# Kernel tuning notes

Measured on AMD Instinct MI355X. Metric: run time of the kernel, lower is better.

Reference implementation:

```python
import jax, jax.numpy as jnp
import numpy as np
import math

DIM = 1024
HEADS = 16
HEAD_DIM = DIM // HEADS
EXPERTS = 8
HIDDEN = 4096  # mlp_ratio * dim
TOP_K = 2
CAP_FACTOR = 1.25
B, S = 2, 2048
CAPACITY = int(math.ceil(B * S * TOP_K * CAP_FACTOR / EXPERTS))  # 1280
EPS = 1e-6


def setup_inputs() -> dict:
    key = jax.random.key(0)
    ks = jax.random.split(key, 16)
    sc_d = 1.0 / math.sqrt(DIM)
    sc_h = 1.0 / math.sqrt(HIDDEN)
    return {
        "x": jax.random.normal(ks[0], (B, S, DIM), jnp.float32),
        "cos": jax.random.uniform(ks[1], (S, HEAD_DIM), jnp.float32),
        "sin": jax.random.uniform(ks[2], (S, HEAD_DIM), jnp.float32),
        "ln1_g": jnp.ones((DIM,), jnp.float32),
        "ln1_b": jnp.zeros((DIM,), jnp.float32),
        "ln2_g": jnp.ones((DIM,), jnp.float32),
        "ln2_b": jnp.zeros((DIM,), jnp.float32),
        "wqkv": jax.random.normal(ks[3], (DIM, 3 * DIM), jnp.float32) * sc_d,
        "bqkv": jnp.zeros((3 * DIM,), jnp.float32),
        "wo": jax.random.normal(ks[4], (DIM, DIM), jnp.float32) * sc_d,
        "bo": jnp.zeros((DIM,), jnp.float32),
        "gate_w": jax.random.normal(ks[5], (DIM, EXPERTS), jnp.float32) * sc_d,
        "w1": jax.random.normal(ks[6], (EXPERTS, DIM, HIDDEN), jnp.float32) * sc_d,
        "b1": jnp.zeros((EXPERTS, HIDDEN), jnp.float32),
        "w2": jax.random.normal(ks[7], (EXPERTS, HIDDEN, DIM), jnp.float32) * sc_h,
        "b2": jnp.zeros((EXPERTS, DIM), jnp.float32),
    }


def _layernorm(x, g, b):
    mu = jnp.mean(x, -1, keepdims=True)
    var = jnp.var(x, -1, keepdims=True)
    return (x - mu) * jax.lax.rsqrt(var + EPS) * g + b


def _rope(t, cos, sin):
    # t: [B, H, S, Dh]; cos/sin: [S, Dh]
    d = t.shape[-1] // 2
    t1, t2 = t[..., :d], t[..., d:]
    rot = jnp.concatenate([-t2, t1], axis=-1)
    return t * cos + rot * sin


def _attention(h, cos, sin, wqkv, bqkv, wo, bo):
    b, s, d = h.shape
    qkv = h @ wqkv + bqkv
    q, k, v = jnp.split(qkv, 3, axis=-1)
    def heads(t):
        return t.reshape(b, s, HEADS, HEAD_DIM).transpose(0, 2, 1, 3)
    q, k, v = heads(q), heads(k), heads(v)
    q = _rope(q, cos, sin)
    k = _rope(k, cos, sin)
    scores = jnp.einsum("bhqd,bhkd->bhqk", q, k) / math.sqrt(HEAD_DIM)
    attn = jax.nn.softmax(scores, axis=-1)
    o = jnp.einsum("bhqk,bhkd->bhqd", attn, v)
    o = o.transpose(0, 2, 1, 3).reshape(b, s, d)
    return o @ wo + bo


def _moe(h, gate_w, w1, b1, w2, b2):
    b, s, d = h.shape
    T = b * s
    xt = h.reshape(T, d)
    probs = jax.nn.softmax(xt @ gate_w, axis=-1)  # [T, E]
    topv, topi = jax.lax.top_k(probs, TOP_K)      # [T, K]
    topw = topv / jnp.sum(topv, -1, keepdims=True)
    # k-major flatten so all first-choice routes get priority
    eid = topi.T.reshape(-1)                      # [K*T]
    wflat = topw.T.reshape(-1)
    tok = jnp.tile(jnp.arange(T), TOP_K)
    oh = jax.nn.one_hot(eid, EXPERTS, dtype=jnp.float32)
    pos = (jnp.cumsum(oh, axis=0) * oh - oh).sum(-1).astype(jnp.int32)
    keep = (pos < CAPACITY).astype(xt.dtype)
    posc = jnp.minimum(pos, CAPACITY - 1)
    buf = jnp.zeros((EXPERTS, CAPACITY, d), xt.dtype).at[eid, posc].add(xt[tok] * keep[:, None])
    hh = jax.nn.gelu(jnp.einsum("ecd,edh->ech", buf, w1) + b1[:, None, :])
    out = jnp.einsum("ech,ehd->ecd", hh, w2) + b2[:, None, :]
    yflat = out[eid, posc] * (wflat * keep)[:, None]
    y = jnp.zeros_like(xt).at[tok].add(yflat)
    # load-balancing aux loss
    me = jnp.mean(probs, axis=0)
    ce = jnp.mean(jax.nn.one_hot(topi, EXPERTS, dtype=jnp.float32).sum(1), axis=0) / TOP_K
    aux = EXPERTS * jnp.sum(me * ce)
    return y.reshape(b, s, d), aux


def reference(x, cos, sin, ln1_g, ln1_b, ln2_g, ln2_b, wqkv, bqkv, wo, bo,
              gate_w, w1, b1, w2, b2):
    h = _layernorm(x, ln1_g, ln1_b)
    x = x + _attention(h, cos, sin, wqkv, bqkv, wo, bo)
    h2 = _layernorm(x, ln2_g, ln2_b)
    y, aux = _moe(h2, gate_w, w1, b1, w2, b2)
    return x + y, aux
```

## Files before the change

kernel.cpp:

```cpp
#include <hip/hip_runtime.h>


typedef unsigned short u16;
typedef short bf16x8 __attribute__((ext_vector_type(8)));
typedef float f32x4 __attribute__((ext_vector_type(4)));
typedef _Float16 f16;
typedef f16 f16x8 __attribute__((ext_vector_type(8)));
typedef f16 f16x4 __attribute__((ext_vector_type(4)));
typedef f16 f16x2 __attribute__((ext_vector_type(2)));

#define T_TOKENS 4096
#define SEQ      2048
#define CAPACITY 1280

__device__ __forceinline__ u16 f2bf(float f) {
  unsigned int u = __float_as_uint(f);
  return (u16)((u + 0x7FFFu + ((u >> 16) & 1u)) >> 16);
}
__device__ __forceinline__ float bf2f(u16 h) {
  return __uint_as_float(((unsigned int)h) << 16);
}
__device__ __forceinline__ float gelu_f(float x) {
  float x3 = x * x * x;
  float t = tanhf(0.7978845608028654f * (x + 0.044715f * x3));
  return 0.5f * x * (1.0f + t);
}

__global__ __launch_bounds__(256) void ln_kernel(
    const float* __restrict__ x, const float* __restrict__ g,
    const float* __restrict__ bt, float* __restrict__ of32,
    u16* __restrict__ obf, f16* __restrict__ oh, f16* __restrict__ ol) {
  const int t = blockIdx.x, tid = threadIdx.x;
  float4 v = ((const float4*)(x + (size_t)t * 1024))[tid];
  float s = v.x + v.y + v.z + v.w;
  float sq = v.x * v.x + v.y * v.y + v.z * v.z + v.w * v.w;
#pragma unroll
  for (int d = 1; d < 64; d <<= 1) {
    s += __shfl_xor(s, d);
    sq += __shfl_xor(sq, d);
  }
  __shared__ float red[8];
  if ((tid & 63) == 0) { red[tid >> 6] = s; red[4 + (tid >> 6)] = sq; }
  __syncthreads();
  s = red[0] + red[1] + red[2] + red[3];
  sq = red[4] + red[5] + red[6] + red[7];
  const float mu = s * (1.0f / 1024.0f);
  const float var = sq * (1.0f / 1024.0f) - mu * mu;
  const float rs = rsqrtf(var + 1e-6f);
  float4 gv = ((const float4*)g)[tid];
  float4 bv = ((const float4*)bt)[tid];
  float4 o;
  o.x = (v.x - mu) * rs * gv.x + bv.x;
  o.y = (v.y - mu) * rs * gv.y + bv.y;
  o.z = (v.z - mu) * rs * gv.z + bv.z;
  o.w = (v.w - mu) * rs * gv.w + bv.w;
  if (of32) ((float4*)(of32 + (size_t)t * 1024))[tid] = o;
  if (obf) {
    ushort4 ob;
    ob.x = f2bf(o.x); ob.y = f2bf(o.y); ob.z = f2bf(o.z); ob.w = f2bf(o.w);
    ((ushort4*)(obf + (size_t)t * 1024))[tid] = ob;
  }
  if (oh) {
    const float f[4] = {o.x, o.y, o.z, o.w};
    f16x4 hv, lv;
#pragma unroll
    for (int i = 0; i < 4; ++i) {
      f16 hi = (f16)f[i];
      hv[i] = hi;
      lv[i] = (f16)(f[i] - (float)hi);
    }
    ((f16x4*)(oh + (size_t)t * 1024))[tid] = hv;
    ((f16x4*)(ol + (size_t)t * 1024))[tid] = lv;
  }
}

__global__ __launch_bounds__(256) void transpose_f32_f16hl(
    const float* __restrict__ in, f16* __restrict__ outh, f16* __restrict__ outl,
    int R, int C) {
  __shared__ float tile[32][33];
  const int c0 = blockIdx.x * 32, r0 = blockIdx.y * 32;
  const int tx = threadIdx.x & 31, ty = threadIdx.x >> 5;
#pragma unroll
  for (int i = 0; i < 32; i += 8)
    tile[ty + i][tx] = in[(size_t)(r0 + ty + i) * C + c0 + tx];
  __syncthreads();
#pragma unroll
  for (int i = 0; i < 32; i += 8) {
    const float v = tile[tx][ty + i];
    const f16 hi = (f16)v;
    const size_t idx = (size_t)(c0 + ty + i) * R + r0 + tx;
    outh[idx] = hi;
    outl[idx] = (f16)(v - (float)hi);
  }
}

template <int EPI>
__global__ __launch_bounds__(256, 2) void gemm_f16x3_bt(
    const f16* __restrict__ Agh, const f16* __restrict__ Agl,
    const f16* __restrict__ Bth, const f16* __restrict__ Btl,
    const float* __restrict__ bias, const float* __restrict__ res,
    float* __restrict__ C, f16* __restrict__ Ch, f16* __restrict__ Cl,
    int M, int N, int K) {
  __shared__ f16 Ah[128 * 40], Al[128 * 40], Bh[128 * 40], Bl[128 * 40];
  const int tid = threadIdx.x, lane = tid & 63, w = tid >> 6;
  const int qd = lane >> 4, ml = lane & 15;
  const int m0 = blockIdx.y * 128, n0 = blockIdx.x * 128;
  const int wm = (w & 1) * 64, wn = (w >> 1) * 64;
  f32x4 acc[4][4] = {};

  const int sr = tid >> 1, sc = (tid & 1) * 16;
  const f16* gAh = Agh + (size_t)(m0 + sr) * K + sc;
  const f16* gAl = Agl + (size_t)(m0 + sr) * K + sc;
  const f16* gBh = Bth + (size_t)(n0 + sr) * K + sc;
  const f16* gBl = Btl + (size_t)(n0 + sr) * K + sc;
  f16* lAh = &Ah[sr * 40 + sc];
  f16* lAl = &Al[sr * 40 + sc];
  f16* lBh = &Bh[sr * 40 + sc];
  f16* lBl = &Bl[sr * 40 + sc];

  for (int k0 = 0; k0 < K; k0 += 32) {
    const uint4 ah0 = *(const uint4*)(gAh + k0);
    const uint4 ah1 = *(const uint4*)(gAh + k0 + 8);
    const uint4 al0 = *(const uint4*)(gAl + k0);
    const uint4 al1 = *(const uint4*)(gAl + k0 + 8);
    const uint4 bh0 = *(const uint4*)(gBh + k0);
    const uint4 bh1 = *(const uint4*)(gBh + k0 + 8);
    const uint4 bl0 = *(const uint4*)(gBl + k0);
    const uint4 bl1 = *(const uint4*)(gBl + k0 + 8);
    __syncthreads();
    *(uint4*)lAh = ah0; *(uint4*)(lAh + 8) = ah1;
    *(uint4*)lAl = al0; *(uint4*)(lAl + 8) = al1;
    *(uint4*)lBh = bh0; *(uint4*)(lBh + 8) = bh1;
    *(uint4*)lBl = bl0; *(uint4*)(lBl + 8) = bl1;
    __syncthreads();
    f16x8 fah[4], fal[4], fbh[4], fbl[4];
#pragma unroll
    for (int i = 0; i < 4; ++i) {
      fah[i] = *(const f16x8*)&Ah[(wm + i * 16 + ml) * 40 + qd * 8];
      fal[i] = *(const f16x8*)&Al[(wm + i * 16 + ml) * 40 + qd * 8];
    }
#pragma unroll
    for (int j = 0; j < 4; ++j) {
      fbh[j] = *(const f16x8*)&Bh[(wn + j * 16 + ml) * 40 + qd * 8];
      fbl[j] = *(const f16x8*)&Bl[(wn + j * 16 + ml) * 40 + qd * 8];
    }
#pragma unroll
    for (int i = 0; i < 4; ++i)
#pragma unroll
      for (int j = 0; j < 4; ++j) {
        acc[i][j] = __builtin_amdgcn_mfma_f32_16x16x32_f16(fah[i], fbh[j], acc[i][j], 0, 0, 0);
        acc[i][j] = __builtin_amdgcn_mfma_f32_16x16x32_f16(fah[i], fbl[j], acc[i][j], 0, 0, 0);
        acc[i][j] = __builtin_amdgcn_mfma_f32_16x16x32_f16(fal[i], fbh[j], acc[i][j], 0, 0, 0);
      }
  }
#pragma unroll
  for (int i = 0; i < 4; ++i) {
    const int rr = m0 + wm + i * 16 + qd * 4;
#pragma unroll
    for (int j = 0; j < 4; ++j) {
      const int cc = n0 + wn + j * 16 + ml;
      const float bb = bias[cc];
#pragma unroll
      for (int p = 0; p < 4; ++p) {
        float v = acc[i][j][p] + bb;
        const size_t idx = (size_t)(rr + p) * N + cc;
        if (EPI == 1) {
          C[idx] = v + res[idx];
        } else {
          const f16 hi = (f16)v;
          Ch[idx] = hi;
          Cl[idx] = (f16)(v - (float)hi);
        }
      }
    }
  }
}

__global__ __launch_bounds__(256) void rope_kernel(
    f16* __restrict__ qh, f16* __restrict__ ql, const float* __restrict__ cosb,
    const float* __restrict__ sinb) {
  const int t = blockIdx.x;
  const int s = t & (SEQ - 1);
  f16* rh = qh + (size_t)t * 3072;
  f16* rl = ql + (size_t)t * 3072;
  const int tid = threadIdx.x;
#pragma unroll
  for (int it = 0; it < 2; ++it) {
    const int p = tid + it * 256;
    const int sec = p >> 8;
    const int rem = p & 255;
    const int hd = rem >> 4, d = (rem & 15) * 2;
    const int col = sec * 1024 + hd * 64 + d;
    const float c1a = cosb[s * 64 + d], s1a = sinb[s * 64 + d];
    const float c1b = cosb[s * 64 + d + 1], s1b = sinb[s * 64 + d + 1];
    const float c2a = cosb[s * 64 + d + 32], s2a = sinb[s * 64 + d + 32];
    const float c2b = cosb[s * 64 + d + 33], s2b = sinb[s * 64 + d + 33];
    const f16x2 ah = *(const f16x2*)(rh + col);
    const f16x2 al = *(const f16x2*)(rl + col);
    const f16x2 bh = *(const f16x2*)(rh + col + 32);
    const f16x2 bl = *(const f16x2*)(rl + col + 32);
    const float a0 = (float)ah[0] + (float)al[0];
    const float a1 = (float)ah[1] + (float)al[1];
    const float b0 = (float)bh[0] + (float)bl[0];
    const float b1 = (float)bh[1] + (float)bl[1];
    float na0 = a0 * c1a - b0 * s1a;
    float na1 = a1 * c1b - b1 * s1b;
    float nb0 = b0 * c2a + a0 * s2a;
    float nb1 = b1 * c2b + a1 * s2b;
    if (sec == 0) { na0 *= 0.125f; na1 *= 0.125f; nb0 *= 0.125f; nb1 *= 0.125f; }
    f16x2 nah, nal, nbh, nbl;
    nah[0] = (f16)na0; nal[0] = (f16)(na0 - (float)nah[0]);
    nah[1] = (f16)na1; nal[1] = (f16)(na1 - (float)nah[1]);
    nbh[0] = (f16)nb0; nbl[0] = (f16)(nb0 - (float)nbh[0]);
    nbh[1] = (f16)nb1; nbl[1] = (f16)(nb1 - (float)nbh[1]);
    *(f16x2*)(rh + col) = nah;
    *(f16x2*)(rl + col) = nal;
    *(f16x2*)(rh + col + 32) = nbh;
    *(f16x2*)(rl + col + 32) = nbl;
  }
}

__global__ __launch_bounds__(256) void attn_mfma(
    const f16* __restrict__ qkvh, const f16* __restrict__ qkvl,
    f16* __restrict__ ogh, f16* __restrict__ ogl) {
  const int bh_ = blockIdx.y, b = bh_ >> 4, h = bh_ & 15;
  const int tid = threadIdx.x, w = tid >> 6, lane = tid & 63;
  const int quad = lane >> 4, ml = lane & 15;
  const int q0 = blockIdx.x * 64;
  const f16* baseh = qkvh + (size_t)b * SEQ * 3072 + h * 64;
  const f16* basel = qkvl + (size_t)b * SEQ * 3072 + h * 64;

  __shared__ f16 Kh[64 * 72], Kl[64 * 72];
  __shared__ f16 Vh[64 * 72], Vl[64 * 72];
  __shared__ f16 Ph[64 * 72], Pl[64 * 72];

  f16x8 qh[2], ql[2];
  {
    const f16* qrh = baseh + (size_t)(q0 + w * 16 + ml) * 3072;
    const f16* qrl = basel + (size_t)(q0 + w * 16 + ml) * 3072;
#pragma unroll
    for (int ks = 0; ks < 2; ++ks) {
      qh[ks] = *(const f16x8*)(qrh + ks * 32 + quad * 8);
      ql[ks] = *(const f16x8*)(qrl + ks * 32 + quad * 8);
    }
  }

  float m_i[4] = {-1e30f, -1e30f, -1e30f, -1e30f};
  float l_i[4] = {0.f, 0.f, 0.f, 0.f};
  f32x4 accO[4] = {};

  const int skey = tid >> 2, scg = (tid & 3) * 16;
  const int sd0 = (tid & 15) * 4, sk0 = (tid >> 4) * 4;

  for (int c0 = 0; c0 < SEQ; c0 += 64) {
    __syncthreads();
    {
      const f16* krh = baseh + 1024 + (size_t)(c0 + skey) * 3072 + scg;
      const f16* krl = basel + 1024 + (size_t)(c0 + skey) * 3072 + scg;
      *(f16x8*)&Kh[skey * 72 + scg] = *(const f16x8*)krh;
      *(f16x8*)&Kh[skey * 72 + scg + 8] = *(const f16x8*)(krh + 8);
      *(f16x8*)&Kl[skey * 72 + scg] = *(const f16x8*)krl;
      *(f16x8*)&Kl[skey * 72 + scg + 8] = *(const f16x8*)(krl + 8);

      f16x4 rvh[4], rvl[4];
#pragma unroll
      for (int i = 0; i < 4; ++i) {
        rvh[i] = *(const f16x4*)(baseh + 2048 + (size_t)(c0 + sk0 + i) * 3072 + sd0);
        rvl[i] = *(const f16x4*)(basel + 2048 + (size_t)(c0 + sk0 + i) * 3072 + sd0);
      }
#pragma unroll
      for (int dd = 0; dd < 4; ++dd) {
        f16x4 vh4, vl4;
#pragma unroll
        for (int i = 0; i < 4; ++i) { vh4[i] = rvh[i][dd]; vl4[i] = rvl[i][dd]; }
        *(f16x4*)&Vh[(sd0 + dd) * 72 + sk0] = vh4;
        *(f16x4*)&Vl[(sd0 + dd) * 72 + sk0] = vl4;
      }
    }
    __syncthreads();

    f32x4 s[4] = {};
#pragma unroll
    for (int ks = 0; ks < 2; ++ks)
#pragma unroll
      for (int j = 0; j < 4; ++j) {
        const f16x8 kh = *(const f16x8*)&Kh[(j * 16 + ml) * 72 + ks * 32 + quad * 8];
        const f16x8 kl = *(const f16x8*)&Kl[(j * 16 + ml) * 72 + ks * 32 + quad * 8];
        s[j] = __builtin_amdgcn_mfma_f32_16x16x32_f16(qh[ks], kh, s[j], 0, 0, 0);
        s[j] = __builtin_amdgcn_mfma_f32_16x16x32_f16(qh[ks], kl, s[j], 0, 0, 0);
        s[j] = __builtin_amdgcn_mfma_f32_16x16x32_f16(ql[ks], kh, s[j], 0, 0, 0);
      }

    float alpha[4];
#pragma unroll
    for (int p = 0; p < 4; ++p) {
      float mx = fmaxf(fmaxf(s[0][p], s[1][p]), fmaxf(s[2][p], s[3][p]));
      mx = fmaxf(mx, __shfl_xor(mx, 1));
      mx = fmaxf(mx, __shfl_xor(mx, 2));
      mx = fmaxf(mx, __shfl_xor(mx, 4));
      mx = fmaxf(mx, __shfl_xor(mx, 8));
      const float mn = fmaxf(m_i[p], mx);
      const float al = __expf(m_i[p] - mn);
      float rs = 0.f;
#pragma unroll
      for (int j = 0; j < 4; ++j) {
        const float e = __expf(s[j][p] - mn);
        s[j][p] = e;
        rs += e;
      }
      rs += __shfl_xor(rs, 1);
      rs += __shfl_xor(rs, 2);
      rs += __shfl_xor(rs, 4);
      rs += __shfl_xor(rs, 8);
      m_i[p] = mn;
      l_i[p] = l_i[p] * al + rs;
      alpha[p] = al;
    }
#pragma unroll
    for (int j = 0; j < 4; ++j)
#pragma unroll
      for (int p = 0; p < 4; ++p) accO[j][p] *= alpha[p];

#pragma unroll
    for (int j = 0; j < 4; ++j)
#pragma unroll
      for (int p = 0; p < 4; ++p) {
        const float v = s[j][p];
        const f16 hi = (f16)v;
        const int row = w * 16 + quad * 4 + p, col = ml + 16 * j;
        Ph[row * 72 + col] = hi;
        Pl[row * 72 + col] = (f16)(v - (float)hi);
      }

#pragma unroll
    for (int ks = 0; ks < 2; ++ks) {
      const f16x8 pah = *(const f16x8*)&Ph[(w * 16 + ml) * 72 + ks * 32 + quad * 8];
      const f16x8 pal = *(const f16x8*)&Pl[(w * 16 + ml) * 72 + ks * 32 + quad * 8];
#pragma unroll
      for (int j = 0; j < 4; ++j) {
        const f16x8 vbh = *(const f16x8*)&Vh[(j * 16 + ml) * 72 + ks * 32 + quad * 8];
        const f16x8 vbl = *(const f16x8*)&Vl[(j * 16 + ml) * 72 + ks * 32 + quad * 8];
        accO[j] = __builtin_amdgcn_mfma_f32_16x16x32_f16(pah, vbh, accO[j], 0, 0, 0);
        accO[j] = __builtin_amdgcn_mfma_f32_16x16x32_f16(pah, vbl, accO[j], 0, 0, 0);
        accO[j] = __builtin_amdgcn_mfma_f32_16x16x32_f16(pal, vbh, accO[j], 0, 0, 0);
      }
    }
  }
  const int trow = q0 + w * 16 + quad * 4;
#pragma unroll
  for (int p = 0; p < 4; ++p) {
    const float inv = 1.0f / l_i[p];
    const size_t ob = (size_t)(b * SEQ + trow + p) * 1024 + h * 64 + ml;
#pragma unroll
    for (int j = 0; j < 4; ++j) {
      const float v = accO[j][p] * inv;
      const f16 hi = (f16)v;
      ogh[ob + j * 16] = hi;
      ogl[ob + j * 16] = (f16)(v - (float)hi);
    }
  }
}

__global__ __launch_bounds__(256) void gate_kernel(
    const float* __restrict__ h2, const float* __restrict__ gw,
    int* __restrict__ topi, float* __restrict__ tw, float* __restrict__ me_part) {
  const int tid = threadIdx.x, w = tid >> 6, lane = tid & 63;
  const int t = blockIdx.x * 4 + w;
  const float* xr = h2 + (size_t)t * 1024;
  float acc[8] = {0.f, 0.f, 0.f, 0.f, 0.f, 0.f, 0.f, 0.f};
#pragma unroll
  for (int i = 0; i < 16; ++i) {
    const int d = lane + i * 64;
    const float xv = xr[d];
    const float4 g0 = ((const float4*)(gw + (size_t)d * 8))[0];
    const float4 g1 = ((const float4*)(gw + (size_t)d * 8))[1];
    acc[0] = fmaf(xv, g0.x, acc[0]); acc[1] = fmaf(xv, g0.y, acc[1]);
    acc[2] = fmaf(xv, g0.z, acc[2]); acc[3] = fmaf(xv, g0.w, acc[3]);
    acc[4] = fmaf(xv, g1.x, acc[4]); acc[5] = fmaf(xv, g1.y, acc[5]);
    acc[6] = fmaf(xv, g1.z, acc[6]); acc[7] = fmaf(xv, g1.w, acc[7]);
  }
#pragma unroll
  for (int e = 0; e < 8; ++e) {
    float v = acc[e];
    v += __shfl_xor(v, 1); v += __shfl_xor(v, 2); v += __shfl_xor(v, 4);
    v += __shfl_xor(v, 8); v += __shfl_xor(v, 16); v += __shfl_xor(v, 32);
    acc[e] = v;
  }
  if (lane == 0) {
    float mx = acc[0];
#pragma unroll
    for (int e = 1; e < 8; ++e) mx = fmaxf(mx, acc[e]);
    float ex[8], ssum = 0.f;
#pragma unroll
    for (int e = 0; e < 8; ++e) { ex[e] = __expf(acc[e] - mx); ssum += ex[e]; }
    const float inv = 1.f / ssum;
    float p[8];
#pragma unroll
    for (int e = 0; e < 8; ++e) p[e] = ex[e] * inv;
    int i1 = 0; float v1 = p[0];
#pragma unroll
    for (int e = 1; e < 8; ++e) if (p[e] > v1) { v1 = p[e]; i1 = e; }
    int i2 = (i1 == 0) ? 1 : 0; float v2 = p[i2];
#pragma unroll
    for (int e = 0; e < 8; ++e) if (e != i1 && p[e] > v2) { v2 = p[e]; i2 = e; }
    const float wn = 1.f / (v1 + v2);
    topi[t] = i1; topi[T_TOKENS + t] = i2;
    tw[t] = v1 * wn; tw[T_TOKENS + t] = v2 * wn;
    float4* mp = (float4*)(me_part + (size_t)t * 8);
    mp[0] = make_float4(p[0], p[1], p[2], p[3]);
    mp[1] = make_float4(p[4], p[5], p[6], p[7]);
  }
}

__global__ __launch_bounds__(256) void route_kernel(
    const int* __restrict__ topi, const float* __restrict__ me_part,
    int* __restrict__ pos, float* __restrict__ aux_out) {
  __shared__ int cnt[256][8];
  __shared__ float fme[256][8];
  __shared__ int tot[8];
  __shared__ float sme[8];
  const int tid = threadIdx.x;
  int lc[8] = {0, 0, 0, 0, 0, 0, 0, 0};
  const int i0 = tid * 32;
  for (int j = 0; j < 32; ++j) lc[topi[i0 + j]]++;
  float fm[8] = {0.f, 0.f, 0.f, 0.f, 0.f, 0.f, 0.f, 0.f};
  for (int r = tid; r < T_TOKENS; r += 256) {
    const float4 p0 = ((const float4*)(me_part + (size_t)r * 8))[0];
    const float4 p1 = ((const float4*)(me_part + (size_t)r * 8))[1];
    fm[0] += p0.x; fm[1] += p0.y; fm[2] += p0.z; fm[3] += p0.w;
    fm[4] += p1.x; fm[5] += p1.y; fm[6] += p1.z; fm[7] += p1.w;
  }
#pragma unroll
  for (int e = 0; e < 8; ++e) { cnt[tid][e] = lc[e]; fme[tid][e] = fm[e]; }
  __syncthreads();
  if (tid < 8) {
    int run = 0;
    float s = 0.f;
    for (int j = 0; j < 256; ++j) {
      const int v = cnt[j][tid];
      cnt[j][tid] = run;
      run += v;
      s += fme[j][tid];
    }
    tot[tid] = run;
    sme[tid] = s;
  }
  __syncthreads();
  int base[8];
#pragma unroll
  for (int e = 0; e < 8; ++e) base[e] = cnt[tid][e];
  for (int j = 0; j < 32; ++j) {
    const int e = topi[i0 + j];
    pos[i0 + j] = base[e]++;
  }
  if (tid == 0) {
    float aux = 0.f;
    for (int e = 0; e < 8; ++e) {
      const float me = sme[e] / 4096.0f;
      const float ce = (float)tot[e] / (4096.0f * 2.0f);
      aux += me * ce;
    }
    aux_out[0] = 8.0f * aux;
  }
}

__global__ __launch_bounds__(128) void moe_scatter(
    const u16* __restrict__ h2b, const int* __restrict__ topi,
    const int* __restrict__ pos, u16* __restrict__ buf) {
  const int i = blockIdx.x;
  const int p = pos[i];
  if (p >= CAPACITY) return;
  const int e = topi[i];
  const int t = i & (T_TOKENS - 1);
  const uint4* src = (const uint4*)(h2b + (size_t)t * 1024);
  uint4* dst = (uint4*)(buf + ((size_t)e * CAPACITY + p) * 1024);
  dst[threadIdx.x] = src[threadIdx.x];
}

__global__ __launch_bounds__(256) void transpose_f32_bf16(
    const float* __restrict__ in, u16* __restrict__ out, int R, int C, long sz) {
  const float* ip = in + (size_t)blockIdx.z * sz;
  u16* op = out + (size_t)blockIdx.z * sz;
  __shared__ float tile[32][33];
  const int c0 = blockIdx.x * 32, r0 = blockIdx.y * 32;
  const int tx = threadIdx.x & 31, ty = threadIdx.x >> 5;
#pragma unroll
  for (int i = 0; i < 32; i += 8)
    tile[ty + i][tx] = ip[(size_t)(r0 + ty + i) * C + c0 + tx];
  __syncthreads();
#pragma unroll
  for (int i = 0; i < 32; i += 8)
    op[(size_t)(c0 + ty + i) * R + r0 + tx] = f2bf(tile[tx][ty + i]);
}

template <int EPI>
__global__ __launch_bounds__(256, 2) void bgemm_bt(
    const u16* __restrict__ Ab, const u16* __restrict__ BTb,
    const float* __restrict__ biasb, u16* __restrict__ Cb,
    int M, int N, int K, long sA, long sB, long sBias, long sC) {
  const int e = blockIdx.z;
  const u16* A = Ab + (size_t)e * sA;
  const u16* BT = BTb + (size_t)e * sB;
  const float* bias = biasb + (size_t)e * sBias;
  u16* C = Cb + (size_t)e * sC;

  __shared__ u16 As[128 * 40];
  __shared__ u16 Bs[128 * 40];
  const int tid = threadIdx.x, lane = tid & 63, w = tid >> 6;
  const int qd = lane >> 4, ml = lane & 15;
  const int m0 = blockIdx.y * 128, n0 = blockIdx.x * 128;
  const int wm = (w & 1) * 64, wn = (w >> 1) * 64;
  f32x4 acc[4][4] = {};

  const int sr = tid >> 1, sh = (tid & 1) * 16;
  const u16* gA = A + (size_t)(m0 + sr) * K + sh;
  const u16* gB = BT + (size_t)(n0 + sr) * K + sh;
  u16* lA = &As[sr * 40 + sh];
  u16* lB = &Bs[sr * 40 + sh];

  for (int k0 = 0; k0 < K; k0 += 32) {
    const uint4 av0 = *(const uint4*)(gA + k0);
    const uint4 av1 = *(const uint4*)(gA + k0 + 8);
    const uint4 bv0 = *(const uint4*)(gB + k0);
    const uint4 bv1 = *(const uint4*)(gB + k0 + 8);
    __syncthreads();
    *(uint4*)lA = av0; *(uint4*)(lA + 8) = av1;
    *(uint4*)lB = bv0; *(uint4*)(lB + 8) = bv1;
    __syncthreads();
    bf16x8 af[4], bfr[4];
#pragma unroll
    for (int i = 0; i < 4; ++i)
      af[i] = *(const bf16x8*)&As[(wm + i * 16 + ml) * 40 + qd * 8];
#pragma unroll
    for (int j = 0; j < 4; ++j)
      bfr[j] = *(const bf16x8*)&Bs[(wn + j * 16 + ml) * 40 + qd * 8];
#pragma unroll
    for (int i = 0; i < 4; ++i)
#pragma unroll
      for (int j = 0; j < 4; ++j)
        acc[i][j] = __builtin_amdgcn_mfma_f32_16x16x32_bf16(af[i], bfr[j], acc[i][j], 0, 0, 0);
  }
#pragma unroll
  for (int i = 0; i < 4; ++i) {
    const int rr = m0 + wm + i * 16 + qd * 4;
#pragma unroll
    for (int j = 0; j < 4; ++j) {
      const int cc = n0 + wn + j * 16 + ml;
      const float bb = bias[cc];
#pragma unroll
      for (int p = 0; p < 4; ++p) {
        float v = acc[i][j][p] + bb;
        if (EPI == 1) v = gelu_f(v);
        C[(size_t)(rr + p) * N + cc] = f2bf(v);
      }
    }
  }
}

__global__ __launch_bounds__(256) void moe_gather(
    const u16* __restrict__ outm, const int* __restrict__ topi,
    const int* __restrict__ pos, const float* __restrict__ tw,
    float* __restrict__ y) {
  const int t = blockIdx.x;
  const int d = threadIdx.x * 4;
  float a0 = 0.f, a1 = 0.f, a2 = 0.f, a3 = 0.f;
#pragma unroll
  for (int k = 0; k < 2; ++k) {
    const int i = k * T_TOKENS + t;
    const int p = pos[i];
    if (p < CAPACITY) {
      const int e = topi[i];
      const float wg = tw[i];
      const ushort4 r = *(const ushort4*)(outm + ((size_t)e * CAPACITY + p) * 1024 + d);
      a0 = fmaf(wg, bf2f(r.x), a0);
      a1 = fmaf(wg, bf2f(r.y), a1);
      a2 = fmaf(wg, bf2f(r.z), a2);
      a3 = fmaf(wg, bf2f(r.w), a3);
    }
  }
  float4* op = (float4*)(y + (size_t)t * 1024 + d);
  float4 cur = *op;
  cur.x += a0; cur.y += a1; cur.z += a2; cur.w += a3;
  *op = cur;
}

static const size_t OFF_TOPI = 0x100;
static const size_t OFF_TW = 0x8100;
static const size_t OFF_POS = 0x10100;
static const size_t OFF_H = 0x20000;
static const size_t OFF_QKV = OFF_H + 0x1000000;
static const size_t OFF_H2F = OFF_QKV + 0x1400000;
static const size_t OFF_H2B = OFF_QKV + 0x3000000;
static const size_t OFF_BUF = OFF_H2B + 0x800000;
static const size_t OFF_WT = OFF_BUF + 0x1400000;
static const size_t OFF_HH = OFF_WT + 0x4000000;
static const size_t WS_NEED = OFF_HH + 0x5000000;

extern "C" void kernel_launch(void* const* d_in, const int* in_sizes, int n_in,
                              void* d_out, int out_size, void* d_ws, size_t ws_size,
                              hipStream_t stream) {
  (void)in_sizes; (void)n_in; (void)out_size;
  if (ws_size < WS_NEED) return;

  const float* x = (const float*)d_in[0];
  const float* cosb = (const float*)d_in[1];
  const float* sinb = (const float*)d_in[2];
  const float* ln1g = (const float*)d_in[3];
  const float* ln1b = (const float*)d_in[4];
  const float* ln2g = (const float*)d_in[5];
  const float* ln2b = (const float*)d_in[6];
  const float* wqkv = (const float*)d_in[7];
  const float* bqkv = (const float*)d_in[8];
  const float* wo = (const float*)d_in[9];
  const float* bo = (const float*)d_in[10];
  const float* gatew = (const float*)d_in[11];
  const float* w1 = (const float*)d_in[12];
  const float* b1 = (const float*)d_in[13];
  const float* w2 = (const float*)d_in[14];
  const float* b2 = (const float*)d_in[15];
  float* out = (float*)d_out;

  char* ws = (char*)d_ws;
  int* topi = (int*)(ws + OFF_TOPI);
  float* tw = (float*)(ws + OFF_TW);
  int* pos = (int*)(ws + OFF_POS);
  f16* h1h = (f16*)(ws + OFF_H);
  f16* h1l = (f16*)(ws + OFF_H + 0x800000);
  f16* oh = h1h;
  f16* ol = h1l;
  f16* qkvh = (f16*)(ws + OFF_QKV);
  f16* qkvl = (f16*)(ws + OFF_QKV + 0x1800000);
  u16* outm = (u16*)(ws + OFF_QKV);
  float* h2f = (float*)(ws + OFF_H2F);
  u16* h2b = (u16*)(ws + OFF_H2B);
  u16* buf = (u16*)(ws + OFF_BUF);
  u16* wt = (u16*)(ws + OFF_WT);
  f16* wqkvTh = (f16*)(ws + OFF_WT);
  f16* wqkvTl = (f16*)(ws + OFF_WT + 0x600000);
  f16* woTh = (f16*)(ws + OFF_WT + 0xC00000);
  f16* woTl = (f16*)(ws + OFF_WT + 0xE00000);
  float* me_part = (float*)(ws + OFF_WT + 0x1000000);
  u16* hh = (u16*)(ws + OFF_HH);

  ln_kernel<<<4096, 256, 0, stream>>>(x, ln1g, ln1b, nullptr, (u16*)nullptr, h1h, h1l);
  transpose_f32_f16hl<<<dim3(96, 32), 256, 0, stream>>>(wqkv, wqkvTh, wqkvTl, 1024, 3072);
  gemm_f16x3_bt<0><<<dim3(24, 32), 256, 0, stream>>>(h1h, h1l, wqkvTh, wqkvTl, bqkv,
                                                     nullptr, nullptr, qkvh, qkvl,
                                                     4096, 3072, 1024);
  rope_kernel<<<4096, 256, 0, stream>>>(qkvh, qkvl, cosb, sinb);
  transpose_f32_f16hl<<<dim3(32, 32), 256, 0, stream>>>(wo, woTh, woTl, 1024, 1024);
  attn_mfma<<<dim3(32, 32), 256, 0, stream>>>(qkvh, qkvl, oh, ol);
  gemm_f16x3_bt<1><<<dim3(8, 32), 256, 0, stream>>>(oh, ol, woTh, woTl, bo, x,
                                                    out, nullptr, nullptr,
                                                    4096, 1024, 1024);
  ln_kernel<<<4096, 256, 0, stream>>>(out, ln2g, ln2b, h2f, h2b, nullptr, nullptr);
  gate_kernel<<<1024, 256, 0, stream>>>(h2f, gatew, topi, tw, me_part);
  route_kernel<<<1, 256, 0, stream>>>(topi, me_part, pos, out + 4194304);

  moe_scatter<<<8192, 128, 0, stream>>>(h2b, topi, pos, buf);
  transpose_f32_bf16<<<dim3(128, 32, 8), 256, 0, stream>>>(w1, wt, 1024, 4096, 1024L * 4096);
  bgemm_bt<1><<<dim3(32, 10, 8), 256, 0, stream>>>(buf, wt, b1, hh, 1280, 4096, 1024,
                                                   1280L * 1024, 4096L * 1024, 4096, 1280L * 4096);
  transpose_f32_bf16<<<dim3(32, 128, 8), 256, 0, stream>>>(w2, wt, 4096, 1024, 4096L * 1024);
  bgemm_bt<0><<<dim3(8, 10, 8), 256, 0, stream>>>(hh, wt, b2, outm, 1280, 1024, 4096,
                                                  1280L * 4096, 1024L * 4096, 1024, 1280L * 1024);
  moe_gather<<<4096, 256, 0, stream>>>(outm, topi, pos, tw, out);
}
```

Before: 1.069 ms.

## Transpose QK^T MFMA, swizzle attention LDS tiles, per-lane softmax stats

The attention kernel swaps the operands of the QK^T MFMA so each lane holds scores for a single query row. Row max and sum then need only two cross-lane shuffles, and the running max and sum become scalars per lane that are redistributed with __shfl for the output rescale. The LDS tiles drop the 72-element row padding in favour of an XOR swizzle, and P is staged per wave as vectorized f16x4 stores. The aim is less shuffle and LDS-store overhead and fewer bank conflicts, in exchange for more index arithmetic and a subtle lane mapping that must be correct.

```diff
diff --git a/kernel.cpp b/kernel.cpp
--- a/kernel.cpp
+++ b/kernel.cpp
@@ -230,9 +230,11 @@
   const f16* baseh = qkvh + (size_t)b * SEQ * 3072 + h * 64;
   const f16* basel = qkvl + (size_t)b * SEQ * 3072 + h * 64;
 
-  __shared__ f16 Kh[64 * 72], Kl[64 * 72];
-  __shared__ f16 Vh[64 * 72], Vl[64 * 72];
-  __shared__ f16 Ph[64 * 72], Pl[64 * 72];
+  __shared__ f16 Kh[64 * 64], Kl[64 * 64];
+  __shared__ f16 Vh[64 * 64], Vl[64 * 64];
+  __shared__ f16 Ph[4][16 * 64], Pl[4][16 * 64];
+
+#define SWZ(r, c) ((c) ^ (((r) & 7) << 3))
 
   f16x8 qh[2], ql[2];
   {
@@ -245,8 +247,7 @@
     }
   }
 
-  float m_i[4] = {-1e30f, -1e30f, -1e30f, -1e30f};
-  float l_i[4] = {0.f, 0.f, 0.f, 0.f};
+  float m_i = -1e30f, l_i = 0.f;
   f32x4 accO[4] = {};
 
   const int skey = tid >> 2, scg = (tid & 3) * 16;
@@ -257,10 +258,10 @@
     {
       const f16* krh = baseh + 1024 + (size_t)(c0 + skey) * 3072 + scg;
       const f16* krl = basel + 1024 + (size_t)(c0 + skey) * 3072 + scg;
-      *(f16x8*)&Kh[skey * 72 + scg] = *(const f16x8*)krh;
-      *(f16x8*)&Kh[skey * 72 + scg + 8] = *(const f16x8*)(krh + 8);
-      *(f16x8*)&Kl[skey * 72 + scg] = *(const f16x8*)krl;
-      *(f16x8*)&Kl[skey * 72 + scg + 8] = *(const f16x8*)(krl + 8);
+      *(f16x8*)&Kh[skey * 64 + SWZ(skey, scg)] = *(const f16x8*)krh;
+      *(f16x8*)&Kh[skey * 64 + SWZ(skey, scg + 8)] = *(const f16x8*)(krh + 8);
+      *(f16x8*)&Kl[skey * 64 + SWZ(skey, scg)] = *(const f16x8*)krl;
+      *(f16x8*)&Kl[skey * 64 + SWZ(skey, scg + 8)] = *(const f16x8*)(krl + 8);
 
       f16x4 rvh[4], rvl[4];
 #pragma unroll
@@ -273,8 +274,9 @@
         f16x4 vh4, vl4;
 #pragma unroll
         for (int i = 0; i < 4; ++i) { vh4[i] = rvh[i][dd]; vl4[i] = rvl[i][dd]; }
-        *(f16x4*)&Vh[(sd0 + dd) * 72 + sk0] = vh4;
-        *(f16x4*)&Vl[(sd0 + dd) * 72 + sk0] = vl4;
+        const int vr = sd0 + dd;
+        *(f16x4*)&Vh[vr * 64 + SWZ(vr, sk0)] = vh4;
+        *(f16x4*)&Vl[vr * 64 + SWZ(vr, sk0)] = vl4;
       }
     }
     __syncthreads();
@@ -284,81 +286,93 @@
     for (int ks = 0; ks < 2; ++ks)
 #pragma unroll
       for (int j = 0; j < 4; ++j) {
-        const f16x8 kh = *(const f16x8*)&Kh[(j * 16 + ml) * 72 + ks * 32 + quad * 8];
-        const f16x8 kl = *(const f16x8*)&Kl[(j * 16 + ml) * 72 + ks * 32 + quad * 8];
-        s[j] = __builtin_amdgcn_mfma_f32_16x16x32_f16(qh[ks], kh, s[j], 0, 0, 0);
-        s[j] = __builtin_amdgcn_mfma_f32_16x16x32_f16(qh[ks], kl, s[j], 0, 0, 0);
-        s[j] = __builtin_amdgcn_mfma_f32_16x16x32_f16(ql[ks], kh, s[j], 0, 0, 0);
-      }
-
-    float alpha[4];
-#pragma unroll
-    for (int p = 0; p < 4; ++p) {
-      float mx = fmaxf(fmaxf(s[0][p], s[1][p]), fmaxf(s[2][p], s[3][p]));
-      mx = fmaxf(mx, __shfl_xor(mx, 1));
-      mx = fmaxf(mx, __shfl_xor(mx, 2));
-      mx = fmaxf(mx, __shfl_xor(mx, 4));
-      mx = fmaxf(mx, __shfl_xor(mx, 8));
-      const float mn = fmaxf(m_i[p], mx);
-      const float al = __expf(m_i[p] - mn);
-      float rs = 0.f;
-#pragma unroll
-      for (int j = 0; j < 4; ++j) {
+        const int kr = j * 16 + ml;
+        const f16x8 kh = *(const f16x8*)&Kh[kr * 64 + SWZ(kr, ks * 32 + quad * 8)];
+        const f16x8 kl = *(const f16x8*)&Kl[kr * 64 + SWZ(kr, ks * 32 + quad * 8)];
+        s[j] = __builtin_amdgcn_mfma_f32_16x16x32_f16(kh, qh[ks], s[j], 0, 0, 0);
+        s[j] = __builtin_amdgcn_mfma_f32_16x16x32_f16(kl, qh[ks], s[j], 0, 0, 0);
+        s[j] = __builtin_amdgcn_mfma_f32_16x16x32_f16(kh, ql[ks], s[j], 0, 0, 0);
+      }
+
+    float pmax = s[0][0];
+#pragma unroll
+    for (int j = 0; j < 4; ++j)
+#pragma unroll
+      for (int p = 0; p < 4; ++p) pmax = fmaxf(pmax, s[j][p]);
+    pmax = fmaxf(pmax, __shfl_xor(pmax, 16));
+    pmax = fmaxf(pmax, __shfl_xor(pmax, 32));
+    const float mn = fmaxf(m_i, pmax);
+    const float al = __expf(m_i - mn);
+    float rs = 0.f;
+#pragma unroll
+    for (int j = 0; j < 4; ++j)
+#pragma unroll
+      for (int p = 0; p < 4; ++p) {
         const float e = __expf(s[j][p] - mn);
         s[j][p] = e;
         rs += e;
       }
-      rs += __shfl_xor(rs, 1);
-      rs += __shfl_xor(rs, 2);
-      rs += __shfl_xor(rs, 4);
-      rs += __shfl_xor(rs, 8);
-      m_i[p] = mn;
-      l_i[p] = l_i[p] * al + rs;
-      alpha[p] = al;
-    }
+    rs += __shfl_xor(rs, 16);
+    rs += __shfl_xor(rs, 32);
+    m_i = mn;
+    l_i = l_i * al + rs;
+
+    float alpha_p[4];
+#pragma unroll
+    for (int p = 0; p < 4; ++p) alpha_p[p] = __shfl(al, 20 * quad + p);
 #pragma unroll
     for (int j = 0; j < 4; ++j)
 #pragma unroll
-      for (int p = 0; p < 4; ++p) accO[j][p] *= alpha[p];
-
-#pragma unroll
-    for (int j = 0; j < 4; ++j)
+      for (int p = 0; p < 4; ++p) accO[j][p] *= alpha_p[p];
+
+#pragma unroll
+    for (int j = 0; j < 4; ++j) {
+      f16x4 h4, l4;
 #pragma unroll
       for (int p = 0; p < 4; ++p) {
-        const float v = s[j][p];
-        const f16 hi = (f16)v;
-        const int row = w * 16 + quad * 4 + p, col = ml + 16 * j;
-        Ph[row * 72 + col] = hi;
-        Pl[row * 72 + col] = (f16)(v - (float)hi);
-      }
+        const f16 hi = (f16)s[j][p];
+        h4[p] = hi;
+        l4[p] = (f16)(s[j][p] - (float)hi);
+      }
+      const int pc = j * 16 + quad * 4;
+      *(f16x4*)&Ph[w][ml * 64 + SWZ(ml, pc)] = h4;
+      *(f16x4*)&Pl[w][ml * 64 + SWZ(ml, pc)] = l4;
+    }
 
 #pragma unroll
     for (int ks = 0; ks < 2; ++ks) {
-      const f16x8 pah = *(const f16x8*)&Ph[(w * 16 + ml) * 72 + ks * 32 + quad * 8];
-      const f16x8 pal = *(const f16x8*)&Pl[(w * 16 + ml) * 72 + ks * 32 + quad * 8];
+      const f16x8 pah = *(const f16x8*)&Ph[w][ml * 64 + SWZ(ml, ks * 32 + quad * 8)];
+      const f16x8 pal = *(const f16x8*)&Pl[w][ml * 64 + SWZ(ml, ks * 32 + quad * 8)];
 #pragma unroll
       for (int j = 0; j < 4; ++j) {
-        const f16x8 vbh = *(const f16x8*)&Vh[(j * 16 + ml) * 72 + ks * 32 + quad * 8];
-        const f16x8 vbl = *(const f16x8*)&Vl[(j * 16 + ml) * 72 + ks * 32 + quad * 8];
+        const int vr = j * 16 + ml;
+        const f16x8 vbh = *(const f16x8*)&Vh[vr * 64 + SWZ(vr, ks * 32 + quad * 8)];
+        const f16x8 vbl = *(const f16x8*)&Vl[vr * 64 + SWZ(vr, ks * 32 + quad * 8)];
         accO[j] = __builtin_amdgcn_mfma_f32_16x16x32_f16(pah, vbh, accO[j], 0, 0, 0);
         accO[j] = __builtin_amdgcn_mfma_f32_16x16x32_f16(pah, vbl, accO[j], 0, 0, 0);
         accO[j] = __builtin_amdgcn_mfma_f32_16x16x32_f16(pal, vbh, accO[j], 0, 0, 0);
       }
     }
   }
+  float linv_p[4];
+  {
+    const float linv = 1.0f / l_i;
+#pragma unroll
+    for (int p = 0; p < 4; ++p) linv_p[p] = __shfl(linv, 20 * quad + p);
+  }
   const int trow = q0 + w * 16 + quad * 4;
 #pragma unroll
   for (int p = 0; p < 4; ++p) {
-    const float inv = 1.0f / l_i[p];
     const size_t ob = (size_t)(b * SEQ + trow + p) * 1024 + h * 64 + ml;
 #pragma unroll
     for (int j = 0; j < 4; ++j) {
-      const float v = accO[j][p] * inv;
+      const float v = accO[j][p] * linv_p[p];
       const f16 hi = (f16)v;
       ogh[ob + j * 16] = hi;
       ogl[ob + j * 16] = (f16)(v - (float)hi);
     }
   }
+#undef SWZ
 }
 
 __global__ __launch_bounds__(256) void gate_kernel(
```

New measurement: 1.037 ms. 1.03x faster.
